# Optimization experiments

Hardware: AMD Instinct MI355X
Metric: run time of the kernel (lower is better)

The kernel has to match this reference:

```python
import jax, jax.numpy as jnp
import numpy as np

DIM, HEADS, HD, FFN = 1536, 12, 128, 8960
B, F, H, W = 1, 4, 20, 32
S = F * H * W          # 2560 latent tokens
L2 = 512               # text context length
EPS = 1e-6


def _ln(x):
    m = jnp.mean(x, -1, keepdims=True)
    v = jnp.mean(jnp.square(x - m), -1, keepdims=True)
    return (x - m) * jax.lax.rsqrt(v + EPS)


def _rms(x, g):
    return x * jax.lax.rsqrt(jnp.mean(jnp.square(x), -1, keepdims=True) + EPS) * g


def _dyn_quant(x):
    # per-token symmetric int8 dynamic activation quantization (A8, dynamic input scale)
    s = jnp.maximum(jnp.max(jnp.abs(x), -1, keepdims=True) / 127.0, 1e-8)
    q = jnp.clip(jnp.round(x / s), -127.0, 127.0)
    return q, s, jnp.sum(q, -1)   # sum_input used for asymmetric-weight zero-point correction


def _quant_w(w):
    # per-output-channel asymmetric int8 weight quantization (weight_sym=False)
    wmin = jnp.min(w, 1, keepdims=True)
    wmax = jnp.max(w, 1, keepdims=True)
    s = jnp.maximum((wmax - wmin) / 255.0, 1e-8)
    zp = jnp.round(-128.0 - wmin / s)
    qw = jnp.clip(jnp.round(w / s) + zp, -128.0, 127.0)
    return qw, s[:, 0], zp[:, 0]


def _w8a8(qx, s_x, sum_qx, w, b):
    # y = s_x * s_w * (qx @ (qw - zp)^T) + b = s_x*s_w*(qx@qw^T - zp*sum(qx)) + b
    qw, sw, zp = _quant_w(w)
    acc = jnp.einsum('bsi,oi->bso', qx, qw) - sum_qx[..., None] * zp
    return acc * s_x * sw + b


def _rope(x, fr, f, h, w):
    # x: [B,S,N,D] with S == f*h*w; fr: [1024, D//2] complex rope table
    Bn, Sn, N, D = x.shape
    c = D // 2
    s0 = c - 2 * (c // 3)
    fF = jnp.broadcast_to(fr[:f, :s0].reshape(f, 1, 1, s0), (f, h, w, s0))
    fH = jnp.broadcast_to(fr[:h, s0:s0 + c // 3].reshape(1, h, 1, c // 3), (f, h, w, c // 3))
    fW = jnp.broadcast_to(fr[:w, s0 + c // 3:].reshape(1, 1, w, c // 3), (f, h, w, c // 3))
    fi = jnp.concatenate([fF, fH, fW], -1).reshape(1, f * h * w, 1, c)
    xr = x.reshape(Bn, Sn, N, c, 2)
    xc = jax.lax.complex(xr[..., 0], xr[..., 1]) * fi
    return jnp.stack([jnp.real(xc), jnp.imag(xc)], -1).reshape(Bn, Sn, N, D)


def _attn(q, k, v, k_lens):
    scale = 1.0 / jnp.sqrt(jnp.float32(q.shape[-1]))
    scores = jnp.einsum('bqnd,bknd->bnqk', q, k) * scale
    mask = jnp.arange(k.shape[1])[None, None, None, :] < k_lens[:, None, None, None]
    p = jax.nn.softmax(jnp.where(mask, scores, -1e30), -1)
    return jnp.einsum('bnqk,bknd->bqnd', p, v)


def _forward(x, e, freqs, context, modulation,
             wq, bq, wk, bk, wv, bv, wo, bo, gq, gk, n3_w, n3_b,
             cwq, cbq, cwk, cbk, cwv, cbv, cwo, cbo, cgq, cgk,
             w1, b1, w2, b2, f, h, w, seq_lens, context_lens):
    fr = jax.lax.complex(freqs[..., 0], freqs[..., 1])
    em = modulation + e  # [B,6,C]
    sm, sc, gm, smlp, scmlp, gmlp = [em[:, i:i + 1] for i in range(6)]
    Bn, Sn, C = x.shape
    # --- self attention: fused norm+modulation then shared per-token int8 quant for q/k/v ---
    h1 = _ln(x) * (1.0 + sc) + sm
    qx, s_x, sum_qx = _dyn_quant(h1)
    q = _rms(_w8a8(qx, s_x, sum_qx, wq, bq), gq).reshape(Bn, Sn, HEADS, HD)
    k = _rms(_w8a8(qx, s_x, sum_qx, wk, bk), gk).reshape(Bn, Sn, HEADS, HD)
    v = _w8a8(qx, s_x, sum_qx, wv, bv).reshape(Bn, Sn, HEADS, HD)
    q = _rope(q, fr, f, h, w)
    k = _rope(k, fr, f, h, w)
    y = _attn(q, k, v, seq_lens).reshape(Bn, Sn, C) @ wo.T + bo
    x = x + y * gm
    # --- cross attention (fp16/fp path in the original; use_kernel[1]=False) ---
    hx = _ln(x) * n3_w + n3_b
    cq = _rms(hx @ cwq.T + cbq, cgq).reshape(Bn, Sn, HEADS, HD)
    ck = _rms(context @ cwk.T + cbk, cgk).reshape(Bn, L2, HEADS, HD)
    cv = (context @ cwv.T + cbv).reshape(Bn, L2, HEADS, HD)
    y = _attn(cq, ck, cv, context_lens).reshape(Bn, Sn, C) @ cwo.T + cbo
    x = x + y
    # --- FFN with modulation (use_kernel[2]=False) ---
    h2 = _ln(x) * (1.0 + scmlp) + smlp
    y = jax.nn.gelu(h2 @ w1.T + b1, approximate=True) @ w2.T + b2
    return x + y * gmlp


def setup_inputs():
    key = jax.random.key(0)
    ks = jax.random.split(key, 16)

    def P(i, shape, s=0.02):
        return jax.random.normal(ks[i], shape, jnp.float32) * s

    x = jax.random.normal(ks[0], (B, S, DIM), jnp.float32)
    e = jax.random.normal(ks[1], (B, 6, DIM), jnp.float32)
    context = jax.random.normal(ks[2], (B, L2, DIM), jnp.float32)
    seq_lens = jnp.array([S], jnp.int32)
    grid_sizes = jnp.array([[F, H, W]], jnp.int32)
    context_lens = jnp.array([L2], jnp.int32)
    c = HD // 2
    pos = np.arange(1024, dtype=np.float64)[:, None]
    theta = 1.0 / (10000.0 ** (np.arange(c, dtype=np.float64) / c))
    ang = pos * theta
    freqs = jnp.asarray(np.stack([np.cos(ang), np.sin(ang)], -1), jnp.float32)
    z = lambda n: jnp.zeros((n,), jnp.float32)
    o = lambda n: jnp.ones((n,), jnp.float32)
    return dict(x=x, e=e, seq_lens=seq_lens, grid_sizes=grid_sizes, freqs=freqs,
                context=context, context_lens=context_lens,
                modulation=P(3, (1, 6, DIM), 1.0 / DIM ** 0.5),
                wq=P(4, (DIM, DIM)), bq=z(DIM), wk=P(5, (DIM, DIM)), bk=z(DIM),
                wv=P(6, (DIM, DIM)), bv=z(DIM), wo=P(7, (DIM, DIM)), bo=z(DIM),
                gq=o(DIM), gk=o(DIM), n3_w=o(DIM), n3_b=z(DIM),
                cwq=P(8, (DIM, DIM)), cbq=z(DIM), cwk=P(9, (DIM, DIM)), cbk=z(DIM),
                cwv=P(10, (DIM, DIM)), cbv=z(DIM), cwo=P(11, (DIM, DIM)), cbo=z(DIM),
                cgq=o(DIM), cgk=o(DIM),
                w1=P(12, (FFN, DIM)), b1=z(FFN), w2=P(13, (DIM, FFN)), b2=z(DIM))


def reference(x, e, seq_lens, grid_sizes, freqs, context, context_lens, modulation,
              wq, bq, wk, bk, wv, bv, wo, bo, gq, gk, n3_w, n3_b,
              cwq, cbq, cwk, cbk, cwv, cbv, cwo, cbo, cgq, cgk,
              w1, b1, w2, b2):
    f, h, w = int(grid_sizes[0, 0]), int(grid_sizes[0, 1]), int(grid_sizes[0, 2])
    return _forward(x, e, freqs, context, modulation,
                    wq, bq, wk, bk, wv, bv, wo, bo, gq, gk, n3_w, n3_b,
                    cwq, cbq, cwk, cbk, cwv, cbv, cwo, cbo, cgq, cgk,
                    w1, b1, w2, b2, f, h, w, seq_lens, context_lens)
```

## Files before the change

### kernel.cpp

```cpp
#include <hip/hip_runtime.h>
#include <stdint.h>


typedef unsigned short u16;
typedef __bf16 bf16x8 __attribute__((ext_vector_type(8)));
typedef float f32x4 __attribute__((ext_vector_type(4)));

#define DEV __device__ __forceinline__

#define WAIT_LGKM0 do { \
  asm volatile("s_waitcnt lgkmcnt(0)" ::: "memory"); \
  __builtin_amdgcn_sched_barrier(0); } while (0)
#define WAIT_VM(N) do { \
  asm volatile("s_waitcnt vmcnt(" #N ")" ::: "memory"); \
  __builtin_amdgcn_sched_barrier(0); } while (0)

DEV u16 f2b(float f) {
  uint32_t u = __float_as_uint(f);
  u += 0x7fffu + ((u >> 16) & 1u);
  return (u16)(u >> 16);
}

DEV float gelu_tanh(float v) {
  float u = 1.5957691216057308f * (v + 0.044715f * v * v * v);
  return v / (1.f + __expf(-u));
}

DEV void gl_lds16(const u16* g, u16* l) {
  __builtin_amdgcn_global_load_lds(
      (const __attribute__((address_space(1))) void*)g,
      (__attribute__((address_space(3))) void*)l, 16, 0, 0);
}

DEV float bred_sum(float v, float* scr) {
  #pragma unroll
  for (int o = 32; o; o >>= 1) v += __shfl_down(v, o, 64);
  if ((threadIdx.x & 63) == 0) scr[threadIdx.x >> 6] = v;
  __syncthreads();
  v = scr[0] + scr[1] + scr[2] + scr[3];
  __syncthreads();
  return v;
}
DEV float bred_max(float v, float* scr) {
  #pragma unroll
  for (int o = 32; o; o >>= 1) v = fmaxf(v, __shfl_down(v, o, 64));
  if ((threadIdx.x & 63) == 0) scr[threadIdx.x >> 6] = v;
  __syncthreads();
  v = fmaxf(fmaxf(scr[0], scr[1]), fmaxf(scr[2], scr[3]));
  __syncthreads();
  return v;
}
DEV float bred_min(float v, float* scr) {
  #pragma unroll
  for (int o = 32; o; o >>= 1) v = fminf(v, __shfl_down(v, o, 64));
  if ((threadIdx.x & 63) == 0) scr[threadIdx.x >> 6] = v;
  __syncthreads();
  v = fminf(fminf(scr[0], scr[1]), fminf(scr[2], scr[3]));
  __syncthreads();
  return v;
}

__global__ __launch_bounds__(256) void pack_kernel(
    const float* __restrict__ e, const float* __restrict__ mod,
    const float* __restrict__ cbk, const float* __restrict__ cbv,
    float* __restrict__ em, float* __restrict__ bckv) {
  int i = blockIdx.x * 256 + threadIdx.x;
  if (i < 9216) em[i] = e[i] + mod[i];
  if (i < 3072) bckv[i] = (i < 1536) ? cbk[i] : cbv[i - 1536];
}

__global__ __launch_bounds__(256) void cvt_bf16_kernel(
    const float* __restrict__ in, u16* __restrict__ out, int n4) {
  int stride = gridDim.x * 256;
  for (int i = blockIdx.x * 256 + threadIdx.x; i < n4; i += stride) {
    float4 v = ((const float4*)in)[i];
    uint2 r;
    r.x = (uint32_t)f2b(v.x) | ((uint32_t)f2b(v.y) << 16);
    r.y = (uint32_t)f2b(v.z) | ((uint32_t)f2b(v.w) << 16);
    ((uint2*)out)[i] = r;
  }
}

__global__ __launch_bounds__(256) void ln_quant_kernel(
    const float* __restrict__ x, const float* __restrict__ em,
    u16* __restrict__ qx, float* __restrict__ sx, float* __restrict__ sumq) {
  __shared__ float scr[4];
  const int row = blockIdx.x, tid = threadIdx.x;
  const float* xr = x + (size_t)row * 1536;
  float v[6], s = 0.f, s2 = 0.f;
  #pragma unroll
  for (int t = 0; t < 6; t++) { v[t] = xr[tid + t * 256]; s += v[t]; s2 += v[t] * v[t]; }
  s = bred_sum(s, scr); s2 = bred_sum(s2, scr);
  float mean = s / 1536.f;
  float var = s2 / 1536.f - mean * mean;
  float inv = rsqrtf(var + 1e-6f);
  float hv[6], amax = 0.f;
  #pragma unroll
  for (int t = 0; t < 6; t++) {
    int i = tid + t * 256;
    hv[t] = (v[t] - mean) * inv * (1.f + em[1536 + i]) + em[i];
    amax = fmaxf(amax, fabsf(hv[t]));
  }
  amax = bred_max(amax, scr);
  float sxv = fmaxf(amax / 127.f, 1e-8f);
  float qs = 0.f;
  #pragma unroll
  for (int t = 0; t < 6; t++) {
    int i = tid + t * 256;
    float q = fminf(fmaxf(rintf(hv[t] / sxv), -127.f), 127.f);
    qs += q;
    qx[(size_t)row * 1536 + i] = f2b(q);
  }
  qs = bred_sum(qs, scr);
  if (tid == 0) { sx[row] = sxv; sumq[row] = qs; }
}

__global__ __launch_bounds__(256) void quantw_kernel(
    const float* __restrict__ wq, const float* __restrict__ wk, const float* __restrict__ wv,
    const float* __restrict__ bq, const float* __restrict__ bk, const float* __restrict__ bv,
    u16* __restrict__ qw, float* __restrict__ sw, float* __restrict__ zp, float* __restrict__ ball) {
  __shared__ float scr[4];
  const int row = blockIdx.x, tid = threadIdx.x;
  const int sel = (row >= 3072) ? 2 : (row >= 1536 ? 1 : 0);
  const int r = row - sel * 1536;
  const float* w = sel == 0 ? wq : (sel == 1 ? wk : wv);
  const float* bb = sel == 0 ? bq : (sel == 1 ? bk : bv);
  const float* wr = w + (size_t)r * 1536;
  float v[6], mn = 1e30f, mx = -1e30f;
  #pragma unroll
  for (int t = 0; t < 6; t++) { v[t] = wr[tid + t * 256]; mn = fminf(mn, v[t]); mx = fmaxf(mx, v[t]); }
  mn = bred_min(mn, scr); mx = bred_max(mx, scr);
  float s = fmaxf((mx - mn) / 255.f, 1e-8f);
  float z = rintf(-128.f - mn / s);
  #pragma unroll
  for (int t = 0; t < 6; t++) {
    int i = tid + t * 256;
    float q = fminf(fmaxf(rintf(v[t] / s) + z, -128.f), 127.f);
    qw[(size_t)row * 1536 + i] = f2b(q);
  }
  if (tid == 0) { sw[row] = s; zp[row] = z; ball[row] = bb[r]; }
}

template<int EP>
DEV void gemm_epilogue(float v, int row, int col, int N, void* Cout,
                       const float* bias, const float* sxp, const float* sumqp,
                       const float* swp, const float* zpp,
                       const float* gp, const float* residp) {
  size_t idx = (size_t)row * N + col;
  if constexpr (EP == 0) {
    ((float*)Cout)[idx] = v + bias[col];
  } else if constexpr (EP == 1) {
    v = (v - sumqp[row] * zpp[col]) * (sxp[row] * swp[col]) + bias[col];
    ((float*)Cout)[idx] = v;
  } else if constexpr (EP == 2) {
    v += bias[col];
    if (gp) v *= gp[col];
    ((float*)Cout)[idx] = v + residp[idx];
  } else if constexpr (EP == 3) {
    ((u16*)Cout)[idx] = f2b(gelu_tanh(v + bias[col]));
  } else {
    ((float*)Cout)[idx] = v;
  }
}

struct PtrQuad { void* p0; void* p1; void* p2; void* p3; };

template<int EP>
__global__ __launch_bounds__(512, 2) void gemm256_bt_kernel(
    const u16* __restrict__ A, const u16* __restrict__ B, PtrQuad pq,
    int N, int K, int KC,
    const float* __restrict__ bias,
    const float* __restrict__ sxp, const float* __restrict__ sumqp,
    const float* __restrict__ swp, const float* __restrict__ zpp) {
  __shared__ __align__(16) u16 As[2][256 * 64];
  __shared__ __align__(16) u16 Bs[2][256 * 64];
  const int tid = threadIdx.x;
  const int wave = tid >> 6, lane = tid & 63;
  const int wm = wave >> 2, wn = wave & 3;
  const int quad = lane >> 4, l16 = lane & 15;

  const int gx = gridDim.x, gy = gridDim.y;
  const int nwg = gx * gy * (int)gridDim.z;
  const int orig = ((int)blockIdx.z * gy + (int)blockIdx.y) * gx + (int)blockIdx.x;
  const int qq = nwg >> 3, rr = nwg & 7, xcd = orig & 7, lin = orig >> 3;
  const int wg = (xcd < rr ? xcd * (qq + 1) : rr * (qq + 1) + (xcd - rr) * qq) + lin;
  const int bx = wg % gx, t2 = wg / gx, by = t2 % gy, bz = t2 / gy;
  const int m0 = by * 256, n0 = bx * 256;

  const u16* Abase = A + (size_t)m0 * K + (size_t)bz * KC;
  const u16* Bbase = B + (size_t)n0 * K + (size_t)bz * KC;

  const u16* ap[4]; const u16* bp[4];
  #pragma unroll
  for (int i = 0; i < 4; i++) {
    int idx = i * 512 + tid;
    int row = idx >> 3;
    int col = ((idx & 7) ^ (row & 7)) * 8;
    ap[i] = Abase + (size_t)row * K + col;
    bp[i] = Bbase + (size_t)row * K + col;
  }

  f32x4 acc[8][4];
  #pragma unroll
  for (int i = 0; i < 8; i++)
    #pragma unroll
    for (int j = 0; j < 4; j++) acc[i][j] = (f32x4){0.f, 0.f, 0.f, 0.f};

  auto stA = [&](int buf, int kt) {
    #pragma unroll
    for (int i = 0; i < 4; i++)
      gl_lds16(ap[i] + (kt << 6), &As[buf][(i * 512 + wave * 64) * 8]);
  };
  auto stB = [&](int buf, int kt) {
    #pragma unroll
    for (int i = 0; i < 4; i++)
      gl_lds16(bp[i] + (kt << 6), &Bs[buf][(i * 512 + wave * 64) * 8]);
  };

  bf16x8 afr[4][2], bfr[2][2];
  auto ldA = [&](int cur, int mh) {
    #pragma unroll
    for (int f = 0; f < 4; f++) {
      int row = wm * 128 + mh * 64 + f * 16 + l16;
      int rx = row & 7;
      #pragma unroll
      for (int kk = 0; kk < 2; kk++)
        afr[f][kk] = *(const bf16x8*)&As[cur][row * 64 + (((kk * 4 + quad) ^ rx) << 3)];
    }
  };
  auto ldB = [&](int cur, int nh) {
    #pragma unroll
    for (int f = 0; f < 2; f++) {
      int row = wn * 64 + nh * 32 + f * 16 + l16;
      int rx = row & 7;
      #pragma unroll
      for (int kk = 0; kk < 2; kk++)
        bfr[f][kk] = *(const bf16x8*)&Bs[cur][row * 64 + (((kk * 4 + quad) ^ rx) << 3)];
    }
  };
  auto mmaQ = [&](int mh, int nh) {
    __builtin_amdgcn_s_setprio(1);
    #pragma unroll
    for (int kk = 0; kk < 2; kk++)
      #pragma unroll
      for (int f = 0; f < 4; f++)
        #pragma unroll
        for (int g = 0; g < 2; g++)
          acc[mh * 4 + f][nh * 2 + g] = __builtin_amdgcn_mfma_f32_16x16x32_bf16(
              afr[f][kk], bfr[g][kk], acc[mh * 4 + f][nh * 2 + g], 0, 0, 0);
    __builtin_amdgcn_s_setprio(0);
  };

  const int nk = KC >> 6;
  stA(0, 0); stB(0, 0);
  if (nk > 1) {
    stA(1, 1); stB(1, 1);
    WAIT_VM(8);
  } else {
    WAIT_VM(0);
  }
  __builtin_amdgcn_s_barrier();

  for (int kt = 0; kt < nk; kt++) {
    const int cur = kt & 1;
    const bool st2 = (kt + 2 < nk);
    ldA(cur, 0); ldB(cur, 0);
    __builtin_amdgcn_s_barrier();
    mmaQ(0, 0);
    __builtin_amdgcn_s_barrier();
    ldB(cur, 1);
    __builtin_amdgcn_s_barrier();
    mmaQ(0, 1);
    __builtin_amdgcn_s_barrier();
    ldA(cur, 1);
    WAIT_LGKM0;
    __builtin_amdgcn_s_barrier();
    if (st2) stA(cur, kt + 2);
    mmaQ(1, 1);
    __builtin_amdgcn_s_barrier();
    ldB(cur, 0);
    WAIT_LGKM0;
    __builtin_amdgcn_s_barrier();
    if (st2) stB(cur, kt + 2);
    mmaQ(1, 0);
    if (kt + 1 < nk) {
      if (st2) { WAIT_VM(8); } else { WAIT_VM(0); }
    }
    __builtin_amdgcn_s_barrier();
  }

  void* Cuse;
  if constexpr (EP == 4)
    Cuse = bz == 0 ? pq.p0 : (bz == 1 ? pq.p1 : (bz == 2 ? pq.p2 : pq.p3));
  else
    Cuse = pq.p0;
  #pragma unroll
  for (int mi = 0; mi < 8; mi++)
    #pragma unroll
    for (int ni = 0; ni < 4; ni++) {
      int col = n0 + wn * 64 + ni * 16 + l16;
      #pragma unroll
      for (int r = 0; r < 4; r++)
        gemm_epilogue<EP>(acc[mi][ni][r], m0 + wm * 128 + mi * 16 + quad * 4 + r, col,
                          N, Cuse, bias, sxp, sumqp, swp, zpp, nullptr, nullptr);
    }
}

template<int EP>
__global__ __launch_bounds__(256) void gemm64_bt_kernel(
    const u16* __restrict__ A, const u16* __restrict__ B,
    void* __restrict__ Cout, void* __restrict__ Cout2, int N, int K, int KC,
    const float* __restrict__ bias,
    const float* __restrict__ sxp, const float* __restrict__ sumqp,
    const float* __restrict__ swp, const float* __restrict__ zpp,
    const float* __restrict__ gp, const float* __restrict__ residp) {
  __shared__ __align__(16) u16 As[2][64 * 64];
  __shared__ __align__(16) u16 Bs[2][128 * 64];
  const int tid = threadIdx.x;
  const int wave = tid >> 6, lane = tid & 63;
  const int wm = wave >> 1, wn = wave & 1;
  const int quad = lane >> 4, l16 = lane & 15;
  const int m0 = blockIdx.y * 64, n0 = blockIdx.x * 128;
  const int kstart = blockIdx.z * KC;

  int arow[2], acol[2], brow[4], bcol[4];
  #pragma unroll
  for (int i = 0; i < 2; i++) {
    int row = (wave * 2 + i) * 8 + (lane >> 3);
    arow[i] = row; acol[i] = (((lane & 7) - (row >> 1)) & 7) * 8;
  }
  #pragma unroll
  for (int i = 0; i < 4; i++) {
    int row = (wave * 4 + i) * 8 + (lane >> 3);
    brow[i] = row; bcol[i] = (((lane & 7) - (row >> 1)) & 7) * 8;
  }

  f32x4 acc[2][4];
  #pragma unroll
  for (int i = 0; i < 2; i++)
    #pragma unroll
    for (int j = 0; j < 4; j++) acc[i][j] = (f32x4){0.f, 0.f, 0.f, 0.f};

  const int nk = KC >> 6;
  auto stage = [&](int buf, int k0) {
    #pragma unroll
    for (int i = 0; i < 2; i++)
      gl_lds16(A + (size_t)(m0 + arow[i]) * K + kstart + k0 + acol[i],
               &As[buf][(wave * 2 + i) * 512]);
    #pragma unroll
    for (int i = 0; i < 4; i++)
      gl_lds16(B + (size_t)(n0 + brow[i]) * K + kstart + k0 + bcol[i],
               &Bs[buf][(wave * 4 + i) * 512]);
  };
  stage(0, 0);
  if (nk > 1) {
    stage(1, 64);
    WAIT_VM(6);
  } else {
    WAIT_VM(0);
  }
  __builtin_amdgcn_s_barrier();

  for (int kt = 0; kt < nk; kt++) {
    const int cur = kt & 1;
    const bool st2 = (kt + 2 < nk);
    bf16x8 af[2][2], bfv[2][4];
    #pragma unroll
    for (int s = 0; s < 2; s++) {
      #pragma unroll
      for (int mi = 0; mi < 2; mi++) {
        int row = wm * 32 + mi * 16 + l16;
        int slot = ((s * 4 + quad) + (row >> 1)) & 7;
        af[s][mi] = *(const bf16x8*)&As[cur][row * 64 + slot * 8];
      }
      #pragma unroll
      for (int ni = 0; ni < 4; ni++) {
        int row = wn * 64 + ni * 16 + l16;
        int slot = ((s * 4 + quad) + (row >> 1)) & 7;
        bfv[s][ni] = *(const bf16x8*)&Bs[cur][row * 64 + slot * 8];
      }
    }
    WAIT_LGKM0;
    __builtin_amdgcn_s_barrier();
    if (st2) stage(cur, (kt + 2) << 6);
    __builtin_amdgcn_s_setprio(1);
    #pragma unroll
    for (int s = 0; s < 2; s++)
      #pragma unroll
      for (int mi = 0; mi < 2; mi++)
        #pragma unroll
        for (int ni = 0; ni < 4; ni++)
          acc[mi][ni] = __builtin_amdgcn_mfma_f32_16x16x32_bf16(af[s][mi], bfv[s][ni], acc[mi][ni], 0, 0, 0);
    __builtin_amdgcn_s_setprio(0);
    if (kt + 1 < nk) {
      if (st2) { WAIT_VM(6); } else { WAIT_VM(0); }
    }
    __builtin_amdgcn_s_barrier();
  }
  void* Cuse = (EP == 4 && blockIdx.z) ? Cout2 : Cout;
  #pragma unroll
  for (int mi = 0; mi < 2; mi++)
    #pragma unroll
    for (int ni = 0; ni < 4; ni++) {
      int col = n0 + wn * 64 + ni * 16 + l16;
      #pragma unroll
      for (int r = 0; r < 4; r++)
        gemm_epilogue<EP>(acc[mi][ni][r], m0 + wm * 32 + mi * 16 + quad * 4 + r, col,
                          N, Cuse, bias, sxp, sumqp, swp, zpp, gp, residp);
    }
}

__global__ __launch_bounds__(256) void splitk_reduce4_kernel(
    const float* __restrict__ P0, const float* __restrict__ P1,
    const float* __restrict__ P2, const float* __restrict__ P3,
    float* __restrict__ out, const float* __restrict__ bias,
    const float* __restrict__ g, const float* __restrict__ resid,
    int N, int n4) {
  int stride = gridDim.x * 256;
  for (int i = blockIdx.x * 256 + threadIdx.x; i < n4; i += stride) {
    float4 a = ((const float4*)P0)[i];
    float4 b = ((const float4*)P1)[i];
    float4 c = ((const float4*)P2)[i];
    float4 d = ((const float4*)P3)[i];
    float4 r = ((const float4*)resid)[i];
    int col = (i * 4) % N;
    float4 o;
    o.x = (a.x + b.x + c.x + d.x + bias[col]) * g[col] + r.x;
    o.y = (a.y + b.y + c.y + d.y + bias[col + 1]) * g[col + 1] + r.y;
    o.z = (a.z + b.z + c.z + d.z + bias[col + 2]) * g[col + 2] + r.z;
    o.w = (a.w + b.w + c.w + d.w + bias[col + 3]) * g[col + 3] + r.w;
    ((float4*)out)[i] = o;
  }
}

__global__ __launch_bounds__(256) void rmsrope_b_kernel(
    const float* __restrict__ qkv, u16* __restrict__ qkvb,
    const float* __restrict__ gq, const float* __restrict__ gk,
    const float* __restrict__ freqs, const int* __restrict__ gsz) {
  __shared__ float scr[4];
  const int row = blockIdx.x, tid = threadIdx.x;
  const float* base = qkv + (size_t)row * 4608;
  u16* ob = qkvb + (size_t)row * 4608;
  const int gh = gsz[1], gw = gsz[2];
  const int hw = gh * gw;
  const int fi = row / hw, rem = row - fi * hw;
  const int hi = rem / gw, wi = rem - hi * gw;
  #pragma unroll
  for (int part = 0; part < 2; part++) {
    const float* p = base + part * 1536;
    u16* o = ob + part * 1536;
    const float* g = part ? gk : gq;
    const float sc = part ? 1.f : 0.08838834764831845f;
    float v[6], s2 = 0.f;
    #pragma unroll
    for (int t = 0; t < 6; t++) { v[t] = p[tid + t * 256]; s2 += v[t] * v[t]; }
    s2 = bred_sum(s2, scr);
    float inv = rsqrtf(s2 / 1536.f + 1e-6f);
    #pragma unroll
    for (int t = 0; t < 3; t++) {
      int pr = tid + t * 256;
      int c = pr & 63;
      int frow = (c < 22) ? fi : (c < 43 ? hi : wi);
      const float* fr = freqs + ((size_t)frow * 64 + c) * 2;
      float cv = fr[0], sv = fr[1];
      float x0 = p[2 * pr] * inv * g[2 * pr];
      float x1 = p[2 * pr + 1] * inv * g[2 * pr + 1];
      o[2 * pr] = f2b((x0 * cv - x1 * sv) * sc);
      o[2 * pr + 1] = f2b((x0 * sv + x1 * cv) * sc);
    }
  }
  #pragma unroll
  for (int t = 0; t < 6; t++) {
    int i = tid + t * 256;
    ob[3072 + i] = f2b(base[3072 + i]);
  }
}

__global__ __launch_bounds__(256) void rms_bf16_kernel(
    const float* __restrict__ X, u16* __restrict__ O, const float* __restrict__ g,
    int ldi, int ldo, float scale) {
  __shared__ float scr[4];
  const int row = blockIdx.x, tid = threadIdx.x;
  const float* xr = X + (size_t)row * ldi;
  u16* orow = O + (size_t)row * ldo;
  float v[6], s2 = 0.f;
  #pragma unroll
  for (int t = 0; t < 6; t++) { v[t] = xr[tid + t * 256]; s2 += v[t] * v[t]; }
  s2 = bred_sum(s2, scr);
  float inv = rsqrtf(s2 / 1536.f + 1e-6f) * scale;
  #pragma unroll
  for (int t = 0; t < 6; t++) {
    int i = tid + t * 256;
    orow[i] = f2b(v[t] * inv * g[i]);
  }
}

__global__ __launch_bounds__(256) void vtrans_kernel(
    const float* __restrict__ V, int ld, u16* __restrict__ Vt, int Skv) {
  __shared__ u16 T[64 * 136];
  const int h = blockIdx.y, k0 = blockIdx.x * 64, tid = threadIdx.x;
  #pragma unroll
  for (int i = 0; i < 8; i++) {
    int f4 = i * 256 + tid;
    int row = f4 >> 5, c4 = f4 & 31;
    float4 v = *(const float4*)(V + (size_t)(k0 + row) * ld + h * 128 + c4 * 4);
    ushort4 b;
    b.x = f2b(v.x); b.y = f2b(v.y); b.z = f2b(v.z); b.w = f2b(v.w);
    *(ushort4*)&T[row * 136 + c4 * 4] = b;
  }
  __syncthreads();
  #pragma unroll
  for (int i = 0; i < 4; i++) {
    int f8 = i * 256 + tid;
    int hd = f8 >> 3, kc = f8 & 7;
    u16 tmp[8];
    #pragma unroll
    for (int j = 0; j < 8; j++) tmp[j] = T[(kc * 8 + j) * 136 + hd];
    *(uint4*)(Vt + ((size_t)h * 128 + hd) * Skv + k0 + kc * 8) = *(const uint4*)tmp;
  }
}

__global__ __launch_bounds__(256) void fattn_kernel(
    const u16* __restrict__ Q, int ldq, const u16* __restrict__ Kg, int ldk,
    const u16* __restrict__ Vtg, u16* __restrict__ O, int ldo,
    const int* __restrict__ klen_ptr, int kmax) {
  __shared__ __align__(16) u16 Qs[64 * 136];
  __shared__ __align__(16) u16 Ks[64 * 136];
  __shared__ __align__(16) u16 Vt[128 * 72];
  __shared__ __align__(16) u16 Pt[4][16 * 72];
  const int tid = threadIdx.x, wave = tid >> 6, lane = tid & 63;
  const int quad = lane >> 4, l16 = lane & 15;
  const int h = blockIdx.y;
  const int q0 = blockIdx.x * 64;
  int klen = klen_ptr[0]; if (klen > kmax) klen = kmax;
  const u16* vbase = Vtg + (size_t)h * 128 * kmax;

  #pragma unroll
  for (int i = 0; i < 4; i++) {
    int c8 = i * 256 + tid;
    int row = c8 >> 4, cc = (c8 & 15) * 8;
    *(uint4*)&Qs[row * 136 + cc] = *(const uint4*)(Q + (size_t)(q0 + row) * ldq + h * 128 + cc);
  }
  __syncthreads();
  bf16x8 qf[4];
  #pragma unroll
  for (int s = 0; s < 4; s++)
    qf[s] = *(const bf16x8*)&Qs[(wave * 16 + l16) * 136 + s * 32 + quad * 8];

  float m_r[4] = {-1e30f, -1e30f, -1e30f, -1e30f};
  float l_r[4] = {0.f, 0.f, 0.f, 0.f};
  f32x4 oacc[8];
  #pragma unroll
  for (int n8 = 0; n8 < 8; n8++) oacc[n8] = (f32x4){0.f, 0.f, 0.f, 0.f};

  const int ktiles = (klen + 63) >> 6;
  for (int kt = 0; kt < ktiles; kt++) {
    const int k0 = kt * 64;
    __syncthreads();
    #pragma unroll
    for (int i = 0; i < 4; i++) {
      int c8 = i * 256 + tid;
      int row = c8 >> 4, cc = (c8 & 15) * 8;
      *(uint4*)&Ks[row * 136 + cc] = *(const uint4*)(Kg + (size_t)(k0 + row) * ldk + h * 128 + cc);
    }
    #pragma unroll
    for (int i = 0; i < 4; i++) {
      int f8 = i * 256 + tid;
      int hd = f8 >> 3, kc = f8 & 7;
      *(uint4*)&Vt[hd * 72 + kc * 8] = *(const uint4*)(vbase + (size_t)hd * kmax + k0 + kc * 8);
    }
    __syncthreads();
    f32x4 sacc[4];
    #pragma unroll
    for (int ni = 0; ni < 4; ni++) sacc[ni] = (f32x4){0.f, 0.f, 0.f, 0.f};
    #pragma unroll
    for (int ni = 0; ni < 4; ni++)
      #pragma unroll
      for (int s = 0; s < 4; s++) {
        bf16x8 kf = *(const bf16x8*)&Ks[(ni * 16 + l16) * 136 + s * 32 + quad * 8];
        sacc[ni] = __builtin_amdgcn_mfma_f32_16x16x32_bf16(qf[s], kf, sacc[ni], 0, 0, 0);
      }
    float alpha_r[4];
    #pragma unroll
    for (int r = 0; r < 4; r++) {
      float mx = -1e30f;
      #pragma unroll
      for (int ni = 0; ni < 4; ni++) {
        int col = k0 + ni * 16 + l16;
        float sv = (col < klen) ? sacc[ni][r] : -1e30f;
        sacc[ni][r] = sv;
        mx = fmaxf(mx, sv);
      }
      #pragma unroll
      for (int off = 1; off < 16; off <<= 1) mx = fmaxf(mx, __shfl_xor(mx, off, 64));
      float mnew = fmaxf(m_r[r], mx);
      float alpha = __expf(m_r[r] - mnew);
      float rsum = 0.f;
      float pv[4];
      #pragma unroll
      for (int ni = 0; ni < 4; ni++) {
        float p = __expf(sacc[ni][r] - mnew);
        pv[ni] = p;
        rsum += p;
      }
      #pragma unroll
      for (int off = 1; off < 16; off <<= 1) rsum += __shfl_xor(rsum, off, 64);
      l_r[r] = l_r[r] * alpha + rsum;
      m_r[r] = mnew;
      alpha_r[r] = alpha;
      #pragma unroll
      for (int ni = 0; ni < 4; ni++)
        Pt[wave][(quad * 4 + r) * 72 + ni * 16 + l16] = f2b(pv[ni]);
    }
    #pragma unroll
    for (int n8 = 0; n8 < 8; n8++)
      #pragma unroll
      for (int r = 0; r < 4; r++) oacc[n8][r] *= alpha_r[r];
    #pragma unroll
    for (int s2 = 0; s2 < 2; s2++) {
      bf16x8 pf = *(const bf16x8*)&Pt[wave][l16 * 72 + s2 * 32 + quad * 8];
      #pragma unroll
      for (int n8 = 0; n8 < 8; n8++) {
        bf16x8 vf = *(const bf16x8*)&Vt[(n8 * 16 + l16) * 72 + s2 * 32 + quad * 8];
        oacc[n8] = __builtin_amdgcn_mfma_f32_16x16x32_bf16(pf, vf, oacc[n8], 0, 0, 0);
      }
    }
  }
  float rl[4];
  #pragma unroll
  for (int r = 0; r < 4; r++) rl[r] = 1.f / l_r[r];
  #pragma unroll
  for (int n8 = 0; n8 < 8; n8++)
    #pragma unroll
    for (int r = 0; r < 4; r++) {
      int row = q0 + wave * 16 + quad * 4 + r;
      O[(size_t)row * ldo + h * 128 + n8 * 16 + l16] = f2b(oacc[n8][r] * rl[r]);
    }
}

__global__ __launch_bounds__(256) void ln_affine_kernel(
    const float* __restrict__ X, u16* __restrict__ O,
    const float* __restrict__ w, const float* __restrict__ b, float addone) {
  __shared__ float scr[4];
  const int row = blockIdx.x, tid = threadIdx.x;
  const float* xr = X + (size_t)row * 1536;
  float v[6], s = 0.f, s2 = 0.f;
  #pragma unroll
  for (int t = 0; t < 6; t++) { v[t] = xr[tid + t * 256]; s += v[t]; s2 += v[t] * v[t]; }
  s = bred_sum(s, scr); s2 = bred_sum(s2, scr);
  float mean = s / 1536.f;
  float inv = rsqrtf(s2 / 1536.f - mean * mean + 1e-6f);
  #pragma unroll
  for (int t = 0; t < 6; t++) {
    int i = tid + t * 256;
    O[(size_t)row * 1536 + i] = f2b((v[t] - mean) * inv * (addone + w[i]) + b[i]);
  }
}

extern "C" void kernel_launch(void* const* d_in, const int* in_sizes, int n_in,
                              void* d_out, int out_size, void* d_ws, size_t ws_size,
                              hipStream_t stream) {
  (void)in_sizes; (void)n_in; (void)out_size; (void)ws_size;
  const int S = 2560, D = 1536, L2C = 512, FF = 8960, ND = 4608, CKV = 3072;

  const float* x = (const float*)d_in[0];
  const float* e = (const float*)d_in[1];
  const int* seq_lens = (const int*)d_in[2];
  const int* grid_sz = (const int*)d_in[3];
  const float* freqs = (const float*)d_in[4];
  const float* context = (const float*)d_in[5];
  const int* ctx_lens = (const int*)d_in[6];
  const float* modulation = (const float*)d_in[7];
  const float* wq = (const float*)d_in[8];  const float* bq = (const float*)d_in[9];
  const float* wk = (const float*)d_in[10]; const float* bk = (const float*)d_in[11];
  const float* wv = (const float*)d_in[12]; const float* bv = (const float*)d_in[13];
  const float* wo = (const float*)d_in[14]; const float* bo = (const float*)d_in[15];
  const float* gq = (const float*)d_in[16]; const float* gk = (const float*)d_in[17];
  const float* n3w = (const float*)d_in[18]; const float* n3b = (const float*)d_in[19];
  const float* cwq = (const float*)d_in[20]; const float* cbq = (const float*)d_in[21];
  const float* cwk = (const float*)d_in[22]; const float* cbk = (const float*)d_in[23];
  const float* cwv = (const float*)d_in[24]; const float* cbv = (const float*)d_in[25];
  const float* cwo = (const float*)d_in[26]; const float* cbo = (const float*)d_in[27];
  const float* cgq = (const float*)d_in[28]; const float* cgk = (const float*)d_in[29];
  const float* w1 = (const float*)d_in[30]; const float* b1 = (const float*)d_in[31];
  const float* w2 = (const float*)d_in[32]; const float* b2 = (const float*)d_in[33];

  char* wsb = (char*)d_ws;
  size_t off = 0;
  auto alloc = [&](size_t bytes) -> void* {
    void* r = wsb + off;
    off += (bytes + 255) & ~(size_t)255;
    return r;
  };
  float* em   = (float*)alloc((size_t)6 * D * 4);
  float* bckv = (float*)alloc((size_t)CKV * 4);
  float* ball = (float*)alloc((size_t)ND * 4);
  float* sx   = (float*)alloc((size_t)S * 4);
  float* sumq = (float*)alloc((size_t)S * 4);
  float* sw   = (float*)alloc((size_t)ND * 4);
  float* zp   = (float*)alloc((size_t)ND * 4);
  u16* qx     = (u16*)alloc((size_t)S * D * 2);
  u16* qw     = (u16*)alloc((size_t)ND * D * 2);
  float* qkv  = (float*)alloc((size_t)S * ND * 4);
  u16* qkvb   = (u16*)alloc((size_t)S * ND * 2);
  u16* attnb  = (u16*)alloc((size_t)S * D * 2);
  u16* hx     = (u16*)alloc((size_t)S * D * 2);
  float* cq   = (float*)alloc((size_t)S * D * 4);
  float* ckv  = (float*)alloc((size_t)L2C * CKV * 4);
  u16* ctxb   = (u16*)alloc((size_t)L2C * D * 2);
  u16* cattn  = (u16*)alloc((size_t)S * D * 2);
  u16* wo_b   = (u16*)alloc((size_t)D * D * 2);
  u16* cwq_b  = (u16*)alloc((size_t)D * D * 2);
  u16* cwkv_b = (u16*)alloc((size_t)2 * D * D * 2);
  u16* cwo_b  = (u16*)alloc((size_t)D * D * 2);
  u16* w1_b   = (u16*)alloc((size_t)FF * D * 2);
  u16* w2_b   = (u16*)alloc((size_t)D * FF * 2);
  u16* h3 = (u16*)qkv;
  u16* h2 = attnb;
  u16* vtg = qw;
  u16* cvtg = qx;
  u16* cqb = hx;
  u16* ckvb = ctxb;
  float* x2 = cq;
  float* x1 = (float*)d_out;
  float* outp = (float*)d_out;
  float* P0 = (float*)qx;
  float* P1 = (float*)qkvb;
  float* P2 = (float*)attnb;
  float* P3 = (float*)cattn;

  auto cvt = [&](const float* in, u16* op, size_t n) {
    int n4 = (int)(n / 4);
    int blocks = (n4 + 255) / 256; if (blocks > 4096) blocks = 4096;
    cvt_bf16_kernel<<<blocks, 256, 0, stream>>>(in, op, n4);
  };

  pack_kernel<<<36, 256, 0, stream>>>(e, modulation, cbk, cbv, em, bckv);
  cvt(wo, wo_b, (size_t)D * D);
  cvt(cwq, cwq_b, (size_t)D * D);
  cvt(cwk, cwkv_b, (size_t)D * D);
  cvt(cwv, cwkv_b + (size_t)D * D, (size_t)D * D);
  cvt(cwo, cwo_b, (size_t)D * D);
  cvt(w1, w1_b, (size_t)FF * D);
  cvt(w2, w2_b, (size_t)D * FF);
  cvt(context, ctxb, (size_t)L2C * D);

  ln_quant_kernel<<<S, 256, 0, stream>>>(x, em, qx, sx, sumq);
  quantw_kernel<<<ND, 256, 0, stream>>>(wq, wk, wv, bq, bk, bv, qw, sw, zp, ball);

  {
    PtrQuad pq{qkv, nullptr, nullptr, nullptr};
    gemm256_bt_kernel<1><<<dim3(ND / 256, S / 256), 512, 0, stream>>>(
        qx, qw, pq, ND, D, D, ball, sx, sumq, sw, zp);
  }

  rmsrope_b_kernel<<<S, 256, 0, stream>>>(qkv, qkvb, gq, gk, freqs, grid_sz);
  vtrans_kernel<<<dim3(S / 64, 12), 256, 0, stream>>>(qkv + 3072, ND, vtg, S);

  fattn_kernel<<<dim3(S / 64, 12), 256, 0, stream>>>(
      qkvb, ND, qkvb + 1536, ND, vtg, attnb, D, seq_lens, S);

  gemm64_bt_kernel<2><<<dim3(D / 128, S / 64), 256, 0, stream>>>(
      attnb, wo_b, x1, nullptr, D, D, D, bo, nullptr, nullptr, nullptr, nullptr, em + 2 * D, x);

  ln_affine_kernel<<<S, 256, 0, stream>>>(x1, hx, n3w, n3b, 0.f);

  gemm64_bt_kernel<0><<<dim3(D / 128, S / 64), 256, 0, stream>>>(
      hx, cwq_b, cq, nullptr, D, D, D, cbq, nullptr, nullptr, nullptr, nullptr, nullptr, nullptr);
  gemm64_bt_kernel<0><<<dim3(CKV / 128, L2C / 64), 256, 0, stream>>>(
      ctxb, cwkv_b, ckv, nullptr, CKV, D, D, bckv, nullptr, nullptr, nullptr, nullptr, nullptr, nullptr);

  rms_bf16_kernel<<<S, 256, 0, stream>>>(cq, cqb, cgq, D, D, 0.08838834764831845f);
  rms_bf16_kernel<<<L2C, 256, 0, stream>>>(ckv, ckvb, cgk, CKV, D, 1.f);
  vtrans_kernel<<<dim3(L2C / 64, 12), 256, 0, stream>>>(ckv + 1536, CKV, cvtg, L2C);

  fattn_kernel<<<dim3(S / 64, 12), 256, 0, stream>>>(
      cqb, D, ckvb, D, cvtg, cattn, D, ctx_lens, L2C);

  gemm64_bt_kernel<2><<<dim3(D / 128, S / 64), 256, 0, stream>>>(
      cattn, cwo_b, x2, nullptr, D, D, D, cbo, nullptr, nullptr, nullptr, nullptr, nullptr, x1);

  ln_affine_kernel<<<S, 256, 0, stream>>>(x2, h2, em + 4 * D, em + 3 * D, 1.f);

  {
    PtrQuad pq{h3, nullptr, nullptr, nullptr};
    gemm256_bt_kernel<3><<<dim3(FF / 256, S / 256), 512, 0, stream>>>(
        h2, w1_b, pq, FF, D, D, b1, nullptr, nullptr, nullptr, nullptr);
  }

  {
    PtrQuad pq{P0, P1, P2, P3};
    gemm256_bt_kernel<4><<<dim3(D / 256, S / 256, 4), 512, 0, stream>>>(
        h3, w2_b, pq, D, FF, FF / 4, nullptr, nullptr, nullptr, nullptr, nullptr);
  }
  splitk_reduce4_kernel<<<960, 256, 0, stream>>>(
      P0, P1, P2, P3, outp, b2, em + 5 * D, x2, D, S * D / 4);
}
```

Baseline: 881.3 us.

## Prefetch K/V tiles into registers with XOR-swizzled LDS and batch weight conversions

The flash-attention kernel now loads the next K and V tiles into registers while it computes on the current tile. It also stores them in LDS with an XOR swizzle instead of padded rows, which is meant to hide global-load latency and avoid bank conflicts. Separately, the eight fp32-to-bf16 conversion launches are merged into one 2D-grid kernel to cut launch overhead. The prefetch costs extra registers, which may reduce occupancy, and the merged conversion uses a fixed 430-block grid per job.

```diff
diff --git a/kernel.cpp b/kernel.cpp
--- a/kernel.cpp
+++ b/kernel.cpp
@@ -69,8 +69,17 @@
   if (i < 3072) bckv[i] = (i < 1536) ? cbk[i] : cbv[i - 1536];
 }
 
-__global__ __launch_bounds__(256) void cvt_bf16_kernel(
-    const float* __restrict__ in, u16* __restrict__ out, int n4) {
+struct CvtJobs {
+  const float* src[8];
+  u16* dst[8];
+  int n4[8];
+};
+
+__global__ __launch_bounds__(256) void cvt_all_kernel(CvtJobs j) {
+  const int y = blockIdx.y;
+  const float* in = j.src[y];
+  u16* out = j.dst[y];
+  const int n4 = j.n4[y];
   int stride = gridDim.x * 256;
   for (int i = blockIdx.x * 256 + threadIdx.x; i < n4; i += stride) {
     float4 v = ((const float4*)in)[i];
@@ -525,8 +534,8 @@
     const u16* __restrict__ Vtg, u16* __restrict__ O, int ldo,
     const int* __restrict__ klen_ptr, int kmax) {
   __shared__ __align__(16) u16 Qs[64 * 136];
-  __shared__ __align__(16) u16 Ks[64 * 136];
-  __shared__ __align__(16) u16 Vt[128 * 72];
+  __shared__ __align__(16) u16 Ks[64 * 128];
+  __shared__ __align__(16) u16 Vt[128 * 64];
   __shared__ __align__(16) u16 Pt[4][16 * 72];
   const int tid = threadIdx.x, wave = tid >> 6, lane = tid & 63;
   const int quad = lane >> 4, l16 = lane & 15;
@@ -535,12 +544,30 @@
   int klen = klen_ptr[0]; if (klen > kmax) klen = kmax;
   const u16* vbase = Vtg + (size_t)h * 128 * kmax;
 
+  int krow[4], kchk[4], vhd[4], vkc[4];
+  #pragma unroll
+  for (int i = 0; i < 4; i++) {
+    int c8 = i * 256 + tid;
+    krow[i] = c8 >> 4; kchk[i] = c8 & 15;
+    vhd[i] = c8 >> 3;  vkc[i] = c8 & 7;
+  }
+  uint4 krg[4], vrg[4];
+  auto loadKV = [&](int k0) {
+    #pragma unroll
+    for (int i = 0; i < 4; i++)
+      krg[i] = *(const uint4*)(Kg + (size_t)(k0 + krow[i]) * ldk + h * 128 + kchk[i] * 8);
+    #pragma unroll
+    for (int i = 0; i < 4; i++)
+      vrg[i] = *(const uint4*)(vbase + (size_t)vhd[i] * kmax + k0 + vkc[i] * 8);
+  };
+
   #pragma unroll
   for (int i = 0; i < 4; i++) {
     int c8 = i * 256 + tid;
     int row = c8 >> 4, cc = (c8 & 15) * 8;
     *(uint4*)&Qs[row * 136 + cc] = *(const uint4*)(Q + (size_t)(q0 + row) * ldq + h * 128 + cc);
   }
+  loadKV(0);
   __syncthreads();
   bf16x8 qf[4];
   #pragma unroll
@@ -558,28 +585,25 @@
     const int k0 = kt * 64;
     __syncthreads();
     #pragma unroll
-    for (int i = 0; i < 4; i++) {
-      int c8 = i * 256 + tid;
-      int row = c8 >> 4, cc = (c8 & 15) * 8;
-      *(uint4*)&Ks[row * 136 + cc] = *(const uint4*)(Kg + (size_t)(k0 + row) * ldk + h * 128 + cc);
-    }
-    #pragma unroll
-    for (int i = 0; i < 4; i++) {
-      int f8 = i * 256 + tid;
-      int hd = f8 >> 3, kc = f8 & 7;
-      *(uint4*)&Vt[hd * 72 + kc * 8] = *(const uint4*)(vbase + (size_t)hd * kmax + k0 + kc * 8);
-    }
+    for (int i = 0; i < 4; i++)
+      *(uint4*)&Ks[krow[i] * 128 + ((kchk[i] ^ (krow[i] & 7)) * 8)] = krg[i];
+    #pragma unroll
+    for (int i = 0; i < 4; i++)
+      *(uint4*)&Vt[vhd[i] * 64 + ((vkc[i] ^ (vhd[i] & 7)) * 8)] = vrg[i];
     __syncthreads();
+    if (kt + 1 < ktiles) loadKV(k0 + 64);
     f32x4 sacc[4];
     #pragma unroll
     for (int ni = 0; ni < 4; ni++) sacc[ni] = (f32x4){0.f, 0.f, 0.f, 0.f};
     #pragma unroll
-    for (int ni = 0; ni < 4; ni++)
+    for (int ni = 0; ni < 4; ni++) {
+      int rx = l16 & 7;
       #pragma unroll
       for (int s = 0; s < 4; s++) {
-        bf16x8 kf = *(const bf16x8*)&Ks[(ni * 16 + l16) * 136 + s * 32 + quad * 8];
+        bf16x8 kf = *(const bf16x8*)&Ks[(ni * 16 + l16) * 128 + (((s * 4 + quad) ^ rx) * 8)];
         sacc[ni] = __builtin_amdgcn_mfma_f32_16x16x32_bf16(qf[s], kf, sacc[ni], 0, 0, 0);
       }
+    }
     float alpha_r[4];
     #pragma unroll
     for (int r = 0; r < 4; r++) {
@@ -621,7 +645,8 @@
       bf16x8 pf = *(const bf16x8*)&Pt[wave][l16 * 72 + s2 * 32 + quad * 8];
       #pragma unroll
       for (int n8 = 0; n8 < 8; n8++) {
-        bf16x8 vf = *(const bf16x8*)&Vt[(n8 * 16 + l16) * 72 + s2 * 32 + quad * 8];
+        int rx = l16 & 7;
+        bf16x8 vf = *(const bf16x8*)&Vt[(n8 * 16 + l16) * 64 + (((s2 * 4 + quad) ^ rx) * 8)];
         oacc[n8] = __builtin_amdgcn_mfma_f32_16x16x32_bf16(pf, vf, oacc[n8], 0, 0, 0);
       }
     }
@@ -729,21 +754,20 @@
   float* P2 = (float*)attnb;
   float* P3 = (float*)cattn;
 
-  auto cvt = [&](const float* in, u16* op, size_t n) {
-    int n4 = (int)(n / 4);
-    int blocks = (n4 + 255) / 256; if (blocks > 4096) blocks = 4096;
-    cvt_bf16_kernel<<<blocks, 256, 0, stream>>>(in, op, n4);
-  };
-
   pack_kernel<<<36, 256, 0, stream>>>(e, modulation, cbk, cbv, em, bckv);
-  cvt(wo, wo_b, (size_t)D * D);
-  cvt(cwq, cwq_b, (size_t)D * D);
-  cvt(cwk, cwkv_b, (size_t)D * D);
-  cvt(cwv, cwkv_b + (size_t)D * D, (size_t)D * D);
-  cvt(cwo, cwo_b, (size_t)D * D);
-  cvt(w1, w1_b, (size_t)FF * D);
-  cvt(w2, w2_b, (size_t)D * FF);
-  cvt(context, ctxb, (size_t)L2C * D);
+
+  {
+    CvtJobs j;
+    j.src[0] = wo;      j.dst[0] = wo_b;                      j.n4[0] = D * D / 4;
+    j.src[1] = cwq;     j.dst[1] = cwq_b;                     j.n4[1] = D * D / 4;
+    j.src[2] = cwk;     j.dst[2] = cwkv_b;                    j.n4[2] = D * D / 4;
+    j.src[3] = cwv;     j.dst[3] = cwkv_b + (size_t)D * D;    j.n4[3] = D * D / 4;
+    j.src[4] = cwo;     j.dst[4] = cwo_b;                     j.n4[4] = D * D / 4;
+    j.src[5] = w1;      j.dst[5] = w1_b;                      j.n4[5] = FF * D / 4;
+    j.src[6] = w2;      j.dst[6] = w2_b;                      j.n4[6] = D * FF / 4;
+    j.src[7] = context; j.dst[7] = ctxb;                      j.n4[7] = L2C * D / 4;
+    cvt_all_kernel<<<dim3(430, 8), 256, 0, stream>>>(j);
+  }
 
   ln_quant_kernel<<<S, 256, 0, stream>>>(x, em, qx, sx, sumq);
   quantw_kernel<<<ND, 256, 0, stream>>>(wq, wk, wv, bq, bk, bv, qw, sw, zp, ball);
```

Measured after the change: 950.5 us. 7.9% more time.
